# Performance work log

Hardware: AMD Instinct MI355X
Metric: run time of the kernel (lower is better)

The kernel has to match this reference:

```python
import jax, jax.numpy as jnp
import numpy as np

# Model dims: E experts, T total routed tokens, D model dim, H expert hidden dim
E, T, D, H = 8, 16384, 2048, 5632


def setup_inputs() -> dict:
    key = jax.random.key(0)
    k1, k2, k3, k4 = jax.random.split(key, 4)
    init_std = 0.02
    x = jax.random.normal(k1, (T, D), dtype=jnp.float32)
    # w1/w3: (num_experts, hidden_dim, dim); w2: (num_experts, dim, hidden_dim)
    w1 = jax.random.normal(k2, (E, H, D), dtype=jnp.float32) * init_std
    w2 = jax.random.normal(k3, (E, D, H), dtype=jnp.float32) * init_std
    w3 = jax.random.normal(k4, (E, H, D), dtype=jnp.float32) * init_std
    # Tokens are pre-sorted by expert; even split so sum == T (no padding path)
    num_tokens_per_expert = jnp.full((E,), T // E, dtype=jnp.int32)
    return {"x": x, "w1": w1, "w2": w2, "w3": w3,
            "num_tokens_per_expert": num_tokens_per_expert}


def reference(x, w1, w2, w3, num_tokens_per_expert):
    """Grouped-GEMM SwiGLU experts: out[t] = silu(x@w1[e].T) * (x@w3[e].T) @ w2[e].T
    where e is the expert owning token t (tokens sorted by expert).
    lax.ragged_dot is the exact grouped-GEMM primitive: lhs (m,k), rhs (g,k,n),
    group_sizes (g,) -> (m,n). Weights are stored as (g, out, in), so swap to (g, in, out),
    matching the torch matmul with transpose(-2, -1).
    """
    groups = num_tokens_per_expert.astype(jnp.int32)
    gate = jax.lax.ragged_dot(x, jnp.swapaxes(w1, 1, 2), groups)   # (T, H)
    up = jax.lax.ragged_dot(x, jnp.swapaxes(w3, 1, 2), groups)     # (T, H)
    h = jax.nn.silu(gate) * up                                      # fused SwiGLU
    out = jax.lax.ragged_dot(h, jnp.swapaxes(w2, 1, 2), groups)    # (T, D)
    return out
```

## Files before the change

kernel.cpp:

```cpp
#include <hip/hip_runtime.h>
#include <hip/hip_bf16.h>


typedef __bf16 bf16x8 __attribute__((ext_vector_type(8)));
typedef float f32x4 __attribute__((ext_vector_type(4)));
typedef unsigned short u16x8 __attribute__((ext_vector_type(8)));

constexpr int E = 8;
constexpr int T = 16384;
constexpr int D = 2048;
constexpr int H = 5632;

#define DEV static __device__ __forceinline__

DEV unsigned short f2bf(float f) {
    unsigned u = __builtin_bit_cast(unsigned, f);
    u = (u + 0x7FFFu + ((u >> 16) & 1u)) >> 16;
    return (unsigned short)u;
}

DEV void gload16(const void* g, void* l) {
    __builtin_amdgcn_global_load_lds(
        (const __attribute__((address_space(1))) void*)g,
        (__attribute__((address_space(3))) void*)l, 16, 0, 0);
}

DEV f32x4 mfma16(bf16x8 a, bf16x8 b, f32x4 c) {
    return __builtin_amdgcn_mfma_f32_16x16x32_bf16(a, b, c, 0, 0, 0);
}

__global__ __launch_bounds__(256) void k_cvt(const float* __restrict__ in,
                                             unsigned short* __restrict__ out,
                                             long n8) {
    long i = (long)blockIdx.x * blockDim.x + threadIdx.x;
    long stride = (long)gridDim.x * blockDim.x;
    for (; i < n8; i += stride) {
        const float4* p = (const float4*)(in + i * 8);
        float4 a = p[0], b = p[1];
        u16x8 r;
        r[0] = f2bf(a.x); r[1] = f2bf(a.y); r[2] = f2bf(a.z); r[3] = f2bf(a.w);
        r[4] = f2bf(b.x); r[5] = f2bf(b.y); r[6] = f2bf(b.z); r[7] = f2bf(b.w);
        *(u16x8*)(out + i * 8) = r;
    }
}

__global__ __launch_bounds__(256) void k_cvt_w13(
    const float* __restrict__ in, unsigned short* __restrict__ out,
    int which) {
    const long n8 = (long)E * H * D / 8;
    long i = (long)blockIdx.x * blockDim.x + threadIdx.x;
    long stride = (long)gridDim.x * blockDim.x;
    for (; i < n8; i += stride) {
        int col8 = (int)(i & 255);
        int row = (int)(i >> 8);
        int e = row / H;
        int h = row - e * H;
        int rr = ((h >> 4) << 5) + (which << 4) + (h & 15);
        const float4* p = (const float4*)(in + i * 8);
        float4 a = p[0], b = p[1];
        u16x8 r;
        r[0] = f2bf(a.x); r[1] = f2bf(a.y); r[2] = f2bf(a.z); r[3] = f2bf(a.w);
        r[4] = f2bf(b.x); r[5] = f2bf(b.y); r[6] = f2bf(b.z); r[7] = f2bf(b.w);
        *(u16x8*)(out + ((size_t)e * (2 * H) + rr) * D + (size_t)col8 * 8) = r;
    }
}

DEV int expert_of_row(const int* __restrict__ ntp, int row0) {
    int e = 0, s = 0;
    for (int i = 0; i < E; ++i) {
        int c = ntp[i];
        if (row0 < s + c) { e = i; break; }
        s += c;
    }
    return e;
}

template <int LDA, int LDB, int NT>
DEV void gemm_core(const unsigned short* pA,
                   const unsigned short* pB,
                   unsigned short* sA, unsigned short* sB, int tid,
                   f32x4 (&acc)[8][4]) {
    const int wid = tid >> 6, lane = tid & 63;
    const int ksl = (((lane >> 4) ^ (lane & 3) ^ ((lane >> 2) & 3)) << 3);
    const int frA = ((wid >> 2) << 7) + (lane & 15);
    const int frB = ((wid & 3) << 6) + (lane & 15);
    const int aoff = frA * 32 + ksl;
    const int boff = frB * 32 + ksl;
    char* ldsA = (char*)sA + wid * 1024;
    char* ldsB = (char*)sB + wid * 1024;

    auto stageA = [&](int t) {
        const unsigned short* g = pA + t * 32;
        char* l = ldsA + (t & 3) * 16384;
        gload16(g, l);
        gload16(g + (size_t)128 * LDA, l + 8192);
    };
    auto stageB = [&](int t) {
        const unsigned short* g = pB + t * 32;
        char* l = ldsB + (t & 3) * 16384;
        gload16(g, l);
        gload16(g + (size_t)128 * LDB, l + 8192);
    };

    stageA(0); stageB(0);
    stageA(1); stageB(1);
    stageA(2); stageB(2);

    for (int t = 0; t < NT; ++t) {
        const int slot = t & 3;
        if (t + 3 < NT) stageA(t + 3);
        const int rem = NT - 1 - t;
        if (rem >= 3)      asm volatile("s_waitcnt vmcnt(10)" ::: "memory");
        else if (rem == 2) asm volatile("s_waitcnt vmcnt(8)" ::: "memory");
        else if (rem == 1) asm volatile("s_waitcnt vmcnt(4)" ::: "memory");
        else               asm volatile("s_waitcnt vmcnt(0)" ::: "memory");
        __builtin_amdgcn_s_barrier();
        __builtin_amdgcn_sched_barrier(0);

        const unsigned short* A = sA + slot * 8192;
        const unsigned short* B = sB + slot * 8192;
        bf16x8 a[4], b[4];
#pragma unroll
        for (int i = 0; i < 4; ++i) a[i] = *(const bf16x8*)&A[aoff + i * 512];
#pragma unroll
        for (int i = 0; i < 4; ++i) b[i] = *(const bf16x8*)&B[boff + i * 512];
        if (t + 3 < NT) stageB(t + 3);
        __builtin_amdgcn_s_setprio(1);
#pragma unroll
        for (int mi = 0; mi < 4; ++mi)
#pragma unroll
            for (int ni = 0; ni < 4; ++ni)
                acc[mi][ni] = mfma16(a[mi], b[ni], acc[mi][ni]);
        __builtin_amdgcn_s_setprio(0);
        __builtin_amdgcn_s_barrier();
#pragma unroll
        for (int i = 0; i < 4; ++i)
            a[i] = *(const bf16x8*)&A[aoff + 2048 + i * 512];
        __builtin_amdgcn_s_setprio(1);
#pragma unroll
        for (int mi = 0; mi < 4; ++mi)
#pragma unroll
            for (int ni = 0; ni < 4; ++ni)
                acc[4 + mi][ni] = mfma16(a[mi], b[ni], acc[4 + mi][ni]);
        __builtin_amdgcn_s_setprio(0);
        __builtin_amdgcn_s_barrier();
    }
}

__global__ __launch_bounds__(512, 2) void k_gate_up(
    const unsigned short* __restrict__ xb,
    const unsigned short* __restrict__ w13b,
    const int* __restrict__ ntp,
    unsigned short* __restrict__ hbuf) {
    __shared__ unsigned short sA[4 * 8192];
    __shared__ unsigned short sB[4 * 8192];

    const int nwg = gridDim.x;
    const int cpx = nwg >> 3;
    const int bid = blockIdx.x;
    const int swz = (bid & 7) * cpx + (bid >> 3);
    const int tm = swz & 63;
    const int tn = swz >> 6;

    const int row0 = tm << 8;
    const int e = expert_of_row(ntp, row0);
    const int tid = threadIdx.x;

    const int srow = tid >> 2;
    const int sslot = (tid & 3) ^ ((tid >> 2) & 3) ^ ((tid >> 4) & 3);
    const unsigned short* pA = xb + (size_t)(row0 + srow) * D + sslot * 8;
    const unsigned short* pB = w13b + (size_t)e * (2 * H) * D +
                               (size_t)((tn << 8) + srow) * D + sslot * 8;

    f32x4 acc[8][4] = {};
    gemm_core<D, D, D / 32>(pA, pB, sA, sB, tid, acc);

    const int wid = tid >> 6, lane = tid & 63;
    const int wm = wid >> 2, wn = wid & 3;
    const int rbase = row0 + (wm << 7) + ((lane >> 4) << 2);
    const int cbase = ((tn << 3) + (wn << 1)) << 4;
#pragma unroll
    for (int mi = 0; mi < 8; ++mi)
#pragma unroll
        for (int pi = 0; pi < 2; ++pi) {
            f32x4 g = acc[mi][2 * pi], u = acc[mi][2 * pi + 1];
            const int hcol = cbase + (pi << 4) + (lane & 15);
#pragma unroll
            for (int j = 0; j < 4; ++j) {
                float gv = g[j];
                float hv = gv * u[j] / (1.f + __expf(-gv));
                hbuf[(size_t)(rbase + (mi << 4) + j) * H + hcol] = f2bf(hv);
            }
        }
}

__global__ __launch_bounds__(512, 2) void k_down(
    const unsigned short* __restrict__ hbuf,
    const unsigned short* __restrict__ w2b,
    const int* __restrict__ ntp,
    float* __restrict__ out) {
    __shared__ unsigned short sA[4 * 8192];
    __shared__ unsigned short sB[4 * 8192];

    const int nwg = gridDim.x;
    const int cpx = nwg >> 3;
    const int bid = blockIdx.x;
    const int swz = (bid & 7) * cpx + (bid >> 3);
    const int tm = swz & 63;
    const int tn = swz >> 6;

    const int row0 = tm << 8;
    const int e = expert_of_row(ntp, row0);
    const int tid = threadIdx.x;

    const int srow = tid >> 2;
    const int sslot = (tid & 3) ^ ((tid >> 2) & 3) ^ ((tid >> 4) & 3);
    const unsigned short* pA = hbuf + (size_t)(row0 + srow) * H + sslot * 8;
    const unsigned short* pB = w2b + (size_t)e * D * H +
                               (size_t)((tn << 8) + srow) * H + sslot * 8;

    f32x4 acc[8][4] = {};
    gemm_core<H, H, H / 32>(pA, pB, sA, sB, tid, acc);

    const int wid = tid >> 6, lane = tid & 63;
    const int wm = wid >> 2, wn = wid & 3;
    const int rbase = row0 + (wm << 7) + ((lane >> 4) << 2);
    const int cb = (tn << 8) + (wn << 6) + (lane & 15);
#pragma unroll
    for (int mi = 0; mi < 8; ++mi)
#pragma unroll
        for (int ni = 0; ni < 4; ++ni) {
            f32x4 c = acc[mi][ni];
#pragma unroll
            for (int j = 0; j < 4; ++j)
                out[(size_t)(rbase + (mi << 4) + j) * D + cb + (ni << 4)] =
                    c[j];
        }
}

extern "C" void kernel_launch(void* const* d_in, const int* in_sizes, int n_in,
                              void* d_out, int out_size, void* d_ws,
                              size_t ws_size, hipStream_t stream) {
    const float* x = (const float*)d_in[0];
    const float* w1 = (const float*)d_in[1];
    const float* w2 = (const float*)d_in[2];
    const float* w3 = (const float*)d_in[3];
    const int* ntp = (const int*)d_in[4];
    float* out = (float*)d_out;

    char* ws = (char*)d_ws;
    unsigned short* xb = (unsigned short*)(ws + 0);
    unsigned short* w13b = (unsigned short*)(ws + 67108864L);
    unsigned short* hbuf = (unsigned short*)(ws + 67108864L + 385875968L);
    unsigned short* w2b = w13b;

    k_cvt<<<2048, 256, 0, stream>>>(x, xb, (long)T * D / 8);
    k_cvt_w13<<<2048, 256, 0, stream>>>(w1, w13b, 0);
    k_cvt_w13<<<2048, 256, 0, stream>>>(w3, w13b, 1);

    k_gate_up<<<(T / 256) * (2 * H / 256), 512, 0, stream>>>(xb, w13b, ntp,
                                                             hbuf);

    k_cvt<<<2048, 256, 0, stream>>>(w2, w2b, (long)E * D * H / 8);

    k_down<<<(T / 256) * (D / 256), 512, 0, stream>>>(hbuf, w2b, ntp, out);
}
```

Before: 1.659 ms.

## Rewrite GEMM core with BK=64 double buffering and four-phase interleaved schedule

Replaces the 4-stage K=32 ring buffer with a 2-stage K=64 double buffer and splits each K-tile into four MFMA phases. Each phase interleaves one quarter of the next tile's global-to-LDS loads with the LDS fragment reads. A new 8-way XOR swizzle spreads the 128-byte rows across LDS banks. The aim is to halve loop iterations and barriers per K and to overlap loads with compute more evenly. The cost is more LDS per stage, a shallower prefetch depth, and fragile hand-tuned vmcnt counts.

```diff
diff --git a/kernel.cpp b/kernel.cpp
--- a/kernel.cpp
+++ b/kernel.cpp
@@ -75,75 +75,141 @@
     return e;
 }
 
-template <int LDA, int LDB, int NT>
-DEV void gemm_core(const unsigned short* pA,
-                   const unsigned short* pB,
-                   unsigned short* sA, unsigned short* sB, int tid,
-                   f32x4 (&acc)[8][4]) {
-    const int wid = tid >> 6, lane = tid & 63;
-    const int ksl = (((lane >> 4) ^ (lane & 3) ^ ((lane >> 2) & 3)) << 3);
-    const int frA = ((wid >> 2) << 7) + (lane & 15);
-    const int frB = ((wid & 3) << 6) + (lane & 15);
-    const int aoff = frA * 32 + ksl;
-    const int boff = frB * 32 + ksl;
-    char* ldsA = (char*)sA + wid * 1024;
-    char* ldsB = (char*)sB + wid * 1024;
-
-    auto stageA = [&](int t) {
-        const unsigned short* g = pA + t * 32;
-        char* l = ldsA + (t & 3) * 16384;
-        gload16(g, l);
-        gload16(g + (size_t)128 * LDA, l + 8192);
+template <int LD_A, int LD_B, int NT>
+DEV void gemm8(const unsigned short* pa, const unsigned short* pb,
+               unsigned short* sA, unsigned short* sB, int tid,
+               f32x4 (&acc)[8][4]) {
+    const int lane = tid & 63, wid = tid >> 6;
+    const int wm = wid >> 2, wn = wid & 3;
+
+    char* lA = (char*)sA;
+    char* lB = (char*)sB;
+    const int dA = wid << 10;
+    const int chunkrow = ((wid >> 2) << 6) + ((wid & 3) << 3);
+    const int dB = chunkrow << 7;
+
+    const int x0 = ((lane >> 4) ^ (lane & 7)) << 3;
+    const int x1 = x0 ^ 32;
+    const int arow = ((wm << 7) + (lane & 15)) << 6;
+    const int brow = ((wn << 6) + (lane & 15)) << 6;
+
+    auto stA1 = [&](int bo) {
+        gload16(pa, lA + bo + dA);
+        gload16(pa + (size_t)128 * LD_A, lA + bo + dA + 16384);
     };
-    auto stageB = [&](int t) {
-        const unsigned short* g = pB + t * 32;
-        char* l = ldsB + (t & 3) * 16384;
-        gload16(g, l);
-        gload16(g + (size_t)128 * LDB, l + 8192);
+    auto stA2 = [&](int bo) {
+        gload16(pa + (size_t)64 * LD_A, lA + bo + dA + 8192);
+        gload16(pa + (size_t)192 * LD_A, lA + bo + dA + 24576);
     };
-
-    stageA(0); stageB(0);
-    stageA(1); stageB(1);
-    stageA(2); stageB(2);
-
-    for (int t = 0; t < NT; ++t) {
-        const int slot = t & 3;
-        if (t + 3 < NT) stageA(t + 3);
-        const int rem = NT - 1 - t;
-        if (rem >= 3)      asm volatile("s_waitcnt vmcnt(10)" ::: "memory");
-        else if (rem == 2) asm volatile("s_waitcnt vmcnt(8)" ::: "memory");
-        else if (rem == 1) asm volatile("s_waitcnt vmcnt(4)" ::: "memory");
-        else               asm volatile("s_waitcnt vmcnt(0)" ::: "memory");
+    auto stB1 = [&](int bo) {
+        gload16(pb, lB + bo + dB);
+        gload16(pb + (size_t)128 * LD_B, lB + bo + dB + 16384);
+    };
+    auto stB2 = [&](int bo) {
+        gload16(pb + (size_t)32 * LD_B, lB + bo + dB + 4096);
+        gload16(pb + (size_t)160 * LD_B, lB + bo + dB + 20480);
+    };
+
+    stA1(0); stB1(0); stB2(0); stA2(0);
+    pa += 64; pb += 64;
+    asm volatile("s_waitcnt vmcnt(4)" ::: "memory");
+    __builtin_amdgcn_s_barrier();
+
+#pragma unroll 1
+    for (int kt = 0; kt < NT; ++kt) {
+        const int bo = (kt & 1) << 15;
+        const int nbo = bo ^ 32768;
+        const bool more = (kt + 1 < NT);
+        const unsigned short* Ab = sA + (bo >> 1) + arow;
+        const unsigned short* Bb = sB + (bo >> 1) + brow;
+        bf16x8 aT[4][2], bT[4][2];
+
+#pragma unroll
+        for (int m = 0; m < 4; ++m) {
+            aT[m][0] = *(const bf16x8*)(Ab + m * 1024 + x0);
+            aT[m][1] = *(const bf16x8*)(Ab + m * 1024 + x1);
+        }
+#pragma unroll
+        for (int n = 0; n < 2; ++n) {
+            bT[n][0] = *(const bf16x8*)(Bb + n * 1024 + x0);
+            bT[n][1] = *(const bf16x8*)(Bb + n * 1024 + x1);
+        }
+        if (more) {
+            stA1(nbo);
+            asm volatile("s_waitcnt vmcnt(4)" ::: "memory");
+        } else {
+            asm volatile("s_waitcnt vmcnt(2)" ::: "memory");
+        }
         __builtin_amdgcn_s_barrier();
         __builtin_amdgcn_sched_barrier(0);
-
-        const unsigned short* A = sA + slot * 8192;
-        const unsigned short* B = sB + slot * 8192;
-        bf16x8 a[4], b[4];
-#pragma unroll
-        for (int i = 0; i < 4; ++i) a[i] = *(const bf16x8*)&A[aoff + i * 512];
-#pragma unroll
-        for (int i = 0; i < 4; ++i) b[i] = *(const bf16x8*)&B[boff + i * 512];
-        if (t + 3 < NT) stageB(t + 3);
         __builtin_amdgcn_s_setprio(1);
 #pragma unroll
-        for (int mi = 0; mi < 4; ++mi)
-#pragma unroll
-            for (int ni = 0; ni < 4; ++ni)
-                acc[mi][ni] = mfma16(a[mi], b[ni], acc[mi][ni]);
+        for (int m = 0; m < 4; ++m)
+#pragma unroll
+            for (int n = 0; n < 2; ++n) {
+                acc[m][n] = mfma16(aT[m][0], bT[n][0], acc[m][n]);
+                acc[m][n] = mfma16(aT[m][1], bT[n][1], acc[m][n]);
+            }
         __builtin_amdgcn_s_setprio(0);
+
+#pragma unroll
+        for (int n = 2; n < 4; ++n) {
+            bT[n][0] = *(const bf16x8*)(Bb + n * 1024 + x0);
+            bT[n][1] = *(const bf16x8*)(Bb + n * 1024 + x1);
+        }
+        if (more) {
+            stB1(nbo);
+            asm volatile("s_waitcnt vmcnt(4)" ::: "memory");
+        } else {
+            asm volatile("s_waitcnt vmcnt(0)" ::: "memory");
+        }
         __builtin_amdgcn_s_barrier();
-#pragma unroll
-        for (int i = 0; i < 4; ++i)
-            a[i] = *(const bf16x8*)&A[aoff + 2048 + i * 512];
+        __builtin_amdgcn_sched_barrier(0);
         __builtin_amdgcn_s_setprio(1);
 #pragma unroll
-        for (int mi = 0; mi < 4; ++mi)
-#pragma unroll
-            for (int ni = 0; ni < 4; ++ni)
-                acc[4 + mi][ni] = mfma16(a[mi], b[ni], acc[4 + mi][ni]);
+        for (int m = 0; m < 4; ++m)
+#pragma unroll
+            for (int n = 2; n < 4; ++n) {
+                acc[m][n] = mfma16(aT[m][0], bT[n][0], acc[m][n]);
+                acc[m][n] = mfma16(aT[m][1], bT[n][1], acc[m][n]);
+            }
         __builtin_amdgcn_s_setprio(0);
+
+#pragma unroll
+        for (int m = 0; m < 4; ++m) {
+            aT[m][0] = *(const bf16x8*)(Ab + 4096 + m * 1024 + x0);
+            aT[m][1] = *(const bf16x8*)(Ab + 4096 + m * 1024 + x1);
+        }
+        if (more) stB2(nbo);
         __builtin_amdgcn_s_barrier();
+        __builtin_amdgcn_sched_barrier(0);
+        __builtin_amdgcn_s_setprio(1);
+#pragma unroll
+        for (int m = 0; m < 4; ++m)
+#pragma unroll
+            for (int n = 2; n < 4; ++n) {
+                acc[4 + m][n] = mfma16(aT[m][0], bT[n][0], acc[4 + m][n]);
+                acc[4 + m][n] = mfma16(aT[m][1], bT[n][1], acc[4 + m][n]);
+            }
+        __builtin_amdgcn_s_setprio(0);
+
+        if (more) {
+            stA2(nbo);
+            asm volatile("s_waitcnt vmcnt(4)" ::: "memory");
+        }
+        __builtin_amdgcn_s_barrier();
+        __builtin_amdgcn_sched_barrier(0);
+        __builtin_amdgcn_s_setprio(1);
+#pragma unroll
+        for (int m = 0; m < 4; ++m)
+#pragma unroll
+            for (int n = 0; n < 2; ++n) {
+                acc[4 + m][n] = mfma16(aT[m][0], bT[n][0], acc[4 + m][n]);
+                acc[4 + m][n] = mfma16(aT[m][1], bT[n][1], acc[4 + m][n]);
+            }
+        __builtin_amdgcn_s_setprio(0);
+
+        pa += 64; pb += 64;
     }
 }
 
@@ -152,8 +218,8 @@
     const unsigned short* __restrict__ w13b,
     const int* __restrict__ ntp,
     unsigned short* __restrict__ hbuf) {
-    __shared__ unsigned short sA[4 * 8192];
-    __shared__ unsigned short sB[4 * 8192];
+    __shared__ unsigned short sA[2 * 16384];
+    __shared__ unsigned short sB[2 * 16384];
 
     const int nwg = gridDim.x;
     const int cpx = nwg >> 3;
@@ -165,26 +231,29 @@
     const int row0 = tm << 8;
     const int e = expert_of_row(ntp, row0);
     const int tid = threadIdx.x;
-
-    const int srow = tid >> 2;
-    const int sslot = (tid & 3) ^ ((tid >> 2) & 3) ^ ((tid >> 4) & 3);
-    const unsigned short* pA = xb + (size_t)(row0 + srow) * D + sslot * 8;
-    const unsigned short* pB = w13b + (size_t)e * (2 * H) * D +
-                               (size_t)((tn << 8) + srow) * D + sslot * 8;
+    const int lane = tid & 63, wid = tid >> 6;
+
+    const int sr = tid >> 3;
+    const int sc = (tid & 7) ^ (sr & 7);
+    const unsigned short* pa = xb + (size_t)(row0 + sr) * D + sc * 8;
+    const int chunkrow = ((wid >> 2) << 6) + ((wid & 3) << 3);
+    const int br = chunkrow + (lane >> 3);
+    const int bc = (lane & 7) ^ (lane >> 3);
+    const unsigned short* pb = w13b + (size_t)e * (2 * H) * D +
+                               (size_t)((tn << 8) + br) * D + bc * 8;
 
     f32x4 acc[8][4] = {};
-    gemm_core<D, D, D / 32>(pA, pB, sA, sB, tid, acc);
-
-    const int wid = tid >> 6, lane = tid & 63;
+    gemm8<D, D, D / 64>(pa, pb, sA, sB, tid, acc);
+
     const int wm = wid >> 2, wn = wid & 3;
     const int rbase = row0 + (wm << 7) + ((lane >> 4) << 2);
-    const int cbase = ((tn << 3) + (wn << 1)) << 4;
+    const int cb = (((tn << 3) + (wn << 1)) << 4) + (lane & 15);
 #pragma unroll
     for (int mi = 0; mi < 8; ++mi)
 #pragma unroll
         for (int pi = 0; pi < 2; ++pi) {
             f32x4 g = acc[mi][2 * pi], u = acc[mi][2 * pi + 1];
-            const int hcol = cbase + (pi << 4) + (lane & 15);
+            const int hcol = cb + (pi << 4);
 #pragma unroll
             for (int j = 0; j < 4; ++j) {
                 float gv = g[j];
@@ -199,8 +268,8 @@
     const unsigned short* __restrict__ w2b,
     const int* __restrict__ ntp,
     float* __restrict__ out) {
-    __shared__ unsigned short sA[4 * 8192];
-    __shared__ unsigned short sB[4 * 8192];
+    __shared__ unsigned short sA[2 * 16384];
+    __shared__ unsigned short sB[2 * 16384];
 
     const int nwg = gridDim.x;
     const int cpx = nwg >> 3;
@@ -212,17 +281,20 @@
     const int row0 = tm << 8;
     const int e = expert_of_row(ntp, row0);
     const int tid = threadIdx.x;
-
-    const int srow = tid >> 2;
-    const int sslot = (tid & 3) ^ ((tid >> 2) & 3) ^ ((tid >> 4) & 3);
-    const unsigned short* pA = hbuf + (size_t)(row0 + srow) * H + sslot * 8;
-    const unsigned short* pB = w2b + (size_t)e * D * H +
-                               (size_t)((tn << 8) + srow) * H + sslot * 8;
+    const int lane = tid & 63, wid = tid >> 6;
+
+    const int sr = tid >> 3;
+    const int sc = (tid & 7) ^ (sr & 7);
+    const unsigned short* pa = hbuf + (size_t)(row0 + sr) * H + sc * 8;
+    const int chunkrow = ((wid >> 2) << 6) + ((wid & 3) << 3);
+    const int br = chunkrow + (lane >> 3);
+    const int bc = (lane & 7) ^ (lane >> 3);
+    const unsigned short* pb = w2b + (size_t)e * D * H +
+                               (size_t)((tn << 8) + br) * H + bc * 8;
 
     f32x4 acc[8][4] = {};
-    gemm_core<H, H, H / 32>(pA, pB, sA, sB, tid, acc);
-
-    const int wid = tid >> 6, lane = tid & 63;
+    gemm8<H, H, H / 64>(pa, pb, sA, sB, tid, acc);
+
     const int wm = wid >> 2, wn = wid & 3;
     const int rbase = row0 + (wm << 7) + ((lane >> 4) << 2);
     const int cb = (tn << 8) + (wn << 6) + (lane & 15);
```

Measured after the change: 1.476 ms. 11.0% less time.

## Restructure GEMM main loop into single-barrier 4-slot ring with new LDS swizzle

Applied to the files above, without the earlier changes.

Replaces the GEMM core with a 4-slot ring pipeline. Each iteration does one barrier, then issues all four A/B global-to-LDS loads for stage t+3. All eight A fragments are loaded at once, where before the M half was split across two barriers. The LDS swizzle and the per-thread staging address mapping change to a row-pair based XOR. The aim is to cut barrier count and sync stalls per K-step, at the cost of more VGPRs for the A fragments and a possible change in LDS bank-conflict behaviour.

```diff
diff --git a/kernel.cpp b/kernel.cpp
--- a/kernel.cpp
+++ b/kernel.cpp
@@ -27,6 +27,15 @@
 
 DEV f32x4 mfma16(bf16x8 a, bf16x8 b, f32x4 c) {
     return __builtin_amdgcn_mfma_f32_16x16x32_bf16(a, b, c, 0, 0, 0);
+}
+
+DEV void cvt8(const float* src, unsigned short* dst) {
+    float4 a = *(const float4*)src;
+    float4 c = *(const float4*)(src + 4);
+    u16x8 r;
+    r[0] = f2bf(a.x); r[1] = f2bf(a.y); r[2] = f2bf(a.z); r[3] = f2bf(a.w);
+    r[4] = f2bf(c.x); r[5] = f2bf(c.y); r[6] = f2bf(c.z); r[7] = f2bf(c.w);
+    *(u16x8*)dst = r;
 }
 
 __global__ __launch_bounds__(256) void k_cvt(const float* __restrict__ in,
@@ -34,14 +43,7 @@
                                              long n8) {
     long i = (long)blockIdx.x * blockDim.x + threadIdx.x;
     long stride = (long)gridDim.x * blockDim.x;
-    for (; i < n8; i += stride) {
-        const float4* p = (const float4*)(in + i * 8);
-        float4 a = p[0], b = p[1];
-        u16x8 r;
-        r[0] = f2bf(a.x); r[1] = f2bf(a.y); r[2] = f2bf(a.z); r[3] = f2bf(a.w);
-        r[4] = f2bf(b.x); r[5] = f2bf(b.y); r[6] = f2bf(b.z); r[7] = f2bf(b.w);
-        *(u16x8*)(out + i * 8) = r;
-    }
+    for (; i < n8; i += stride) cvt8(in + i * 8, out + i * 8);
 }
 
 __global__ __launch_bounds__(256) void k_cvt_w13(
@@ -56,12 +58,8 @@
         int e = row / H;
         int h = row - e * H;
         int rr = ((h >> 4) << 5) + (which << 4) + (h & 15);
-        const float4* p = (const float4*)(in + i * 8);
-        float4 a = p[0], b = p[1];
-        u16x8 r;
-        r[0] = f2bf(a.x); r[1] = f2bf(a.y); r[2] = f2bf(a.z); r[3] = f2bf(a.w);
-        r[4] = f2bf(b.x); r[5] = f2bf(b.y); r[6] = f2bf(b.z); r[7] = f2bf(b.w);
-        *(u16x8*)(out + ((size_t)e * (2 * H) + rr) * D + (size_t)col8 * 8) = r;
+        cvt8(in + i * 8,
+             out + ((size_t)e * (2 * H) + rr) * D + (size_t)col8 * 8);
     }
 }
 
@@ -75,75 +73,61 @@
     return e;
 }
 
-template <int LDA, int LDB, int NT>
-DEV void gemm_core(const unsigned short* pA,
-                   const unsigned short* pB,
-                   unsigned short* sA, unsigned short* sB, int tid,
-                   f32x4 (&acc)[8][4]) {
-    const int wid = tid >> 6, lane = tid & 63;
-    const int ksl = (((lane >> 4) ^ (lane & 3) ^ ((lane >> 2) & 3)) << 3);
-    const int frA = ((wid >> 2) << 7) + (lane & 15);
-    const int frB = ((wid & 3) << 6) + (lane & 15);
-    const int aoff = frA * 32 + ksl;
-    const int boff = frB * 32 + ksl;
-    char* ldsA = (char*)sA + wid * 1024;
-    char* ldsB = (char*)sB + wid * 1024;
-
-    auto stageA = [&](int t) {
-        const unsigned short* g = pA + t * 32;
-        char* l = ldsA + (t & 3) * 16384;
-        gload16(g, l);
-        gload16(g + (size_t)128 * LDA, l + 8192);
+template <int LD, int NT>
+DEV void gemm_ring4(const unsigned short* pa, const unsigned short* pb,
+                    unsigned short* sA, unsigned short* sB, int tid,
+                    f32x4 (&acc)[8][4]) {
+    const int lane = tid & 63, wid = tid >> 6;
+    const int wm = wid >> 2, wn = wid & 3;
+
+    const int q = lane >> 4;
+    const int ar = wm * 128 + (lane & 15);
+    const int a0 = ar * 32 + ((q ^ ((ar >> 1) & 3)) << 3);
+    const int br = wn * 64 + (lane & 15);
+    const int b0 = br * 32 + ((q ^ ((br >> 1) & 3)) << 3);
+
+    char* ldsA = (char*)sA;
+    char* ldsB = (char*)sB;
+    const int dW = wid << 10;
+
+    auto stage = [&](int t) {
+        const int so = (t & 3) << 14;
+        const unsigned short* ga = pa + t * 32;
+        const unsigned short* gb = pb + t * 32;
+        gload16(ga, ldsA + so + dW);
+        gload16(ga + (size_t)128 * LD, ldsA + so + dW + 8192);
+        gload16(gb, ldsB + so + dW);
+        gload16(gb + (size_t)128 * LD, ldsB + so + dW + 8192);
     };
-    auto stageB = [&](int t) {
-        const unsigned short* g = pB + t * 32;
-        char* l = ldsB + (t & 3) * 16384;
-        gload16(g, l);
-        gload16(g + (size_t)128 * LDB, l + 8192);
-    };
-
-    stageA(0); stageB(0);
-    stageA(1); stageB(1);
-    stageA(2); stageB(2);
-
+
+    stage(0); stage(1); stage(2);
+
+#pragma unroll 1
     for (int t = 0; t < NT; ++t) {
-        const int slot = t & 3;
-        if (t + 3 < NT) stageA(t + 3);
-        const int rem = NT - 1 - t;
-        if (rem >= 3)      asm volatile("s_waitcnt vmcnt(10)" ::: "memory");
-        else if (rem == 2) asm volatile("s_waitcnt vmcnt(8)" ::: "memory");
-        else if (rem == 1) asm volatile("s_waitcnt vmcnt(4)" ::: "memory");
-        else               asm volatile("s_waitcnt vmcnt(0)" ::: "memory");
+        if (t < NT - 2)       asm volatile("s_waitcnt vmcnt(8)" ::: "memory");
+        else if (t == NT - 2) asm volatile("s_waitcnt vmcnt(4)" ::: "memory");
+        else                  asm volatile("s_waitcnt vmcnt(0)" ::: "memory");
         __builtin_amdgcn_s_barrier();
         __builtin_amdgcn_sched_barrier(0);
-
-        const unsigned short* A = sA + slot * 8192;
-        const unsigned short* B = sB + slot * 8192;
-        bf16x8 a[4], b[4];
-#pragma unroll
-        for (int i = 0; i < 4; ++i) a[i] = *(const bf16x8*)&A[aoff + i * 512];
-#pragma unroll
-        for (int i = 0; i < 4; ++i) b[i] = *(const bf16x8*)&B[boff + i * 512];
-        if (t + 3 < NT) stageB(t + 3);
+        if (t + 3 < NT) stage(t + 3);
+
+        const unsigned short* A = sA + ((t & 3) << 13) + a0;
+        const unsigned short* B = sB + ((t & 3) << 13) + b0;
+        bf16x8 a[8], b[4];
+#pragma unroll
+        for (int mi = 0; mi < 8; ++mi)
+            a[mi] = *(const bf16x8*)(A + mi * 512);
+#pragma unroll
+        for (int ni = 0; ni < 4; ++ni)
+            b[ni] = *(const bf16x8*)(B + ni * 512);
+
         __builtin_amdgcn_s_setprio(1);
 #pragma unroll
-        for (int mi = 0; mi < 4; ++mi)
+        for (int mi = 0; mi < 8; ++mi)
 #pragma unroll
             for (int ni = 0; ni < 4; ++ni)
                 acc[mi][ni] = mfma16(a[mi], b[ni], acc[mi][ni]);
         __builtin_amdgcn_s_setprio(0);
-        __builtin_amdgcn_s_barrier();
-#pragma unroll
-        for (int i = 0; i < 4; ++i)
-            a[i] = *(const bf16x8*)&A[aoff + 2048 + i * 512];
-        __builtin_amdgcn_s_setprio(1);
-#pragma unroll
-        for (int mi = 0; mi < 4; ++mi)
-#pragma unroll
-            for (int ni = 0; ni < 4; ++ni)
-                acc[4 + mi][ni] = mfma16(a[mi], b[ni], acc[4 + mi][ni]);
-        __builtin_amdgcn_s_setprio(0);
-        __builtin_amdgcn_s_barrier();
     }
 }
 
@@ -165,26 +149,26 @@
     const int row0 = tm << 8;
     const int e = expert_of_row(ntp, row0);
     const int tid = threadIdx.x;
-
-    const int srow = tid >> 2;
-    const int sslot = (tid & 3) ^ ((tid >> 2) & 3) ^ ((tid >> 4) & 3);
-    const unsigned short* pA = xb + (size_t)(row0 + srow) * D + sslot * 8;
-    const unsigned short* pB = w13b + (size_t)e * (2 * H) * D +
-                               (size_t)((tn << 8) + srow) * D + sslot * 8;
+    const int lane = tid & 63, wid = tid >> 6;
+
+    const int srow = wid * 16 + (lane >> 2);
+    const int sq = (lane & 3) ^ ((lane >> 3) & 3);
+    const unsigned short* pa = xb + (size_t)(row0 + srow) * D + sq * 8;
+    const unsigned short* pb = w13b + (size_t)e * (2 * H) * D +
+                               (size_t)((tn << 8) + srow) * D + sq * 8;
 
     f32x4 acc[8][4] = {};
-    gemm_core<D, D, D / 32>(pA, pB, sA, sB, tid, acc);
-
-    const int wid = tid >> 6, lane = tid & 63;
+    gemm_ring4<D, D / 32>(pa, pb, sA, sB, tid, acc);
+
     const int wm = wid >> 2, wn = wid & 3;
     const int rbase = row0 + (wm << 7) + ((lane >> 4) << 2);
-    const int cbase = ((tn << 3) + (wn << 1)) << 4;
+    const int cb = (((tn << 3) + (wn << 1)) << 4) + (lane & 15);
 #pragma unroll
     for (int mi = 0; mi < 8; ++mi)
 #pragma unroll
         for (int pi = 0; pi < 2; ++pi) {
             f32x4 g = acc[mi][2 * pi], u = acc[mi][2 * pi + 1];
-            const int hcol = cbase + (pi << 4) + (lane & 15);
+            const int hcol = cb + (pi << 4);
 #pragma unroll
             for (int j = 0; j < 4; ++j) {
                 float gv = g[j];
@@ -212,17 +196,17 @@
     const int row0 = tm << 8;
     const int e = expert_of_row(ntp, row0);
     const int tid = threadIdx.x;
-
-    const int srow = tid >> 2;
-    const int sslot = (tid & 3) ^ ((tid >> 2) & 3) ^ ((tid >> 4) & 3);
-    const unsigned short* pA = hbuf + (size_t)(row0 + srow) * H + sslot * 8;
-    const unsigned short* pB = w2b + (size_t)e * D * H +
-                               (size_t)((tn << 8) + srow) * H + sslot * 8;
+    const int lane = tid & 63, wid = tid >> 6;
+
+    const int srow = wid * 16 + (lane >> 2);
+    const int sq = (lane & 3) ^ ((lane >> 3) & 3);
+    const unsigned short* pa = hbuf + (size_t)(row0 + srow) * H + sq * 8;
+    const unsigned short* pb = w2b + (size_t)e * D * H +
+                               (size_t)((tn << 8) + srow) * H + sq * 8;
 
     f32x4 acc[8][4] = {};
-    gemm_core<H, H, H / 32>(pA, pB, sA, sB, tid, acc);
-
-    const int wid = tid >> 6, lane = tid & 63;
+    gemm_ring4<H, H / 32>(pa, pb, sA, sB, tid, acc);
+
     const int wm = wid >> 2, wn = wid & 3;
     const int rbase = row0 + (wm << 7) + ((lane >> 4) << 2);
     const int cb = (tn << 8) + (wn << 6) + (lane & 15);
```

New measurement: 1.829 ms. 10.2% more time.
